# Kernel tuning notes

Hardware: AMD Instinct MI355X
Metric: run time of the kernel (lower is better)

## Reference

```python
import jax, jax.numpy as jnp
import numpy as np

EPS = 1e-06
H, D_MODEL = 16, 1024
DK = D_MODEL // H
B, S = 16, 4096


def elu_fea_map(x):
    return jax.nn.elu(x) + 1.0


def setup_inputs() -> dict:
    key = jax.random.key(0)
    ks = jax.random.split(key, 11)
    lim = 1.0 / np.sqrt(D_MODEL)
    u = lambda k, shp: jax.random.uniform(k, shp, jnp.float32, -lim, lim)
    return {
        "query": jax.random.normal(ks[0], (B, D_MODEL), jnp.float32),
        "key": jax.random.normal(ks[1], (B, S, D_MODEL), jnp.float32),
        "value": jax.random.normal(ks[2], (B, S, D_MODEL), jnp.float32),
        "Wq": u(ks[3], (D_MODEL, D_MODEL)), "bq": u(ks[4], (D_MODEL,)),
        "Wk": u(ks[5], (D_MODEL, D_MODEL)), "bk": u(ks[6], (D_MODEL,)),
        "Wv": u(ks[7], (D_MODEL, D_MODEL)), "bv": u(ks[8], (D_MODEL,)),
        "Wo": u(ks[9], (D_MODEL, D_MODEL)), "bo": u(ks[10], (D_MODEL,)),
    }


def reference(query, key, value, Wq, bq, Wk, bk, Wv, bv, Wo, bo):
    nb = query.shape[0]
    # projections; torch Linear: x @ W.T + b
    q = (query @ Wq.T + bq).reshape(nb, 1, H, DK)   # [B,1,H,D]
    k = (key @ Wk.T + bk).reshape(nb, -1, H, DK)    # [B,S,H,D]
    v = (value @ Wv.T + bv).reshape(nb, -1, H, DK)  # [B,S,H,M]
    Q = elu_fea_map(q)
    K = elu_fea_map(k)
    KV = jnp.einsum('bshd,bshm->bhdm', K, v)                      # [B,H,D,M]
    Z = 1.0 / (jnp.einsum('bshd,bhd->bsh', Q, K.sum(axis=1)) + EPS)  # [B,1,H]
    V = jnp.einsum('bshd,bhdm,bsh->bshm', Q, KV, Z)               # [B,1,H,M]
    x = V.reshape(nb, H * DK)
    return x @ Wo.T + bo
```

## Files before the change

### kernel.cpp

```cpp
#include <hip/hip_runtime.h>
#include <hip/hip_bf16.h>
#include <stdint.h>


using bf16 = __hip_bfloat16;
typedef __attribute__((ext_vector_type(8))) short short8;
typedef __attribute__((ext_vector_type(4))) float f32x4;

#define NB_B 16
#define SEQ 4096
#define DM 1024
#define NH 16
#define DKH 64

__device__ __forceinline__ void gload_lds16(const void* g, void* l) {
  __builtin_amdgcn_global_load_lds((const __attribute__((address_space(1))) void*)g,
                                   (__attribute__((address_space(3))) void*)l, 16, 0, 0);
}

__device__ __forceinline__ short8 pack_bf16x8(float4 a, float4 b) {
  union { bf16 h[8]; short8 v; } pk;
  pk.h[0] = __float2bfloat16(a.x); pk.h[1] = __float2bfloat16(a.y);
  pk.h[2] = __float2bfloat16(a.z); pk.h[3] = __float2bfloat16(a.w);
  pk.h[4] = __float2bfloat16(b.x); pk.h[5] = __float2bfloat16(b.y);
  pk.h[6] = __float2bfloat16(b.z); pk.h[7] = __float2bfloat16(b.w);
  return pk.v;
}

__global__ __launch_bounds__(256) void conv_kernel(const float* __restrict__ src,
                                                   bf16* __restrict__ dst, long n4) {
  long i = (long)blockIdx.x * blockDim.x + threadIdx.x;
  const long stride = (long)gridDim.x * blockDim.x;
  for (; i < n4; i += stride) {
    float4 v = ((const float4*)src)[i];
    union { ushort4 u; bf16 h[4]; } o;
    o.h[0] = __float2bfloat16(v.x);
    o.h[1] = __float2bfloat16(v.y);
    o.h[2] = __float2bfloat16(v.z);
    o.h[3] = __float2bfloat16(v.w);
    ((ushort4*)dst)[i] = o.u;
  }
}

template <int KPROJ>
__global__ __launch_bounds__(256) void gemm_proj(
    const float* __restrict__ A, const bf16* __restrict__ W,
    const float* __restrict__ bias, bf16* __restrict__ outT,
    float* __restrict__ Ksum, int rowsTot, int b0, int chunk) {
  __shared__ bf16 As[2][128 * 64];
  __shared__ bf16 Bs[2][128 * 64];
  const int tid = threadIdx.x;
  const int lane = tid & 63;
  const int wid = tid >> 6;
  const int wr = wid >> 1, wc = wid & 1;
  const int wgid = (blockIdx.x & 7) * chunk + (blockIdx.x >> 3);
  const int row0 = (wgid >> 3) * 128;
  const int col0 = (wgid & 7) * 128;
  f32x4 acc[4][4] = {};

  const int str = tid >> 3;
  const int sslotA = ((tid & 7) ^ (str & 7)) << 4;
  const int acol = (tid & 7) * 8;
  const int bsrc = ((lane & 7) ^ (lane >> 3)) * 8;
  const int xr = (lane & 7) << 4;
  const int lr = lane & 15;
  const int lk = (lane >> 4) * 16;

  const float* Arow[4];
#pragma unroll
  for (int i = 0; i < 4; ++i) Arow[i] = A + (long)(row0 + i * 32 + str) * DM + acol;
  const bf16* Wrow = W + (long)(col0 + wid * 32 + (lane >> 3)) * DM + bsrc;

  float4 fa[4][2];
#pragma unroll
  for (int i = 0; i < 4; ++i) {
    fa[i][0] = *(const float4*)(Arow[i]);
    fa[i][1] = *(const float4*)(Arow[i] + 4);
  }
#pragma unroll
  for (int i = 0; i < 4; ++i)
    gload_lds16(Wrow + i * 8 * DM, &Bs[0][(wid * 4 + i) * 512]);
#pragma unroll
  for (int i = 0; i < 4; ++i)
    *(short8*)((char*)As[0] + (i * 32 + str) * 128 + sslotA) = pack_bf16x8(fa[i][0], fa[i][1]);
#pragma unroll
  for (int i = 0; i < 4; ++i) {
    fa[i][0] = *(const float4*)(Arow[i] + 64);
    fa[i][1] = *(const float4*)(Arow[i] + 68);
  }
  asm volatile("s_waitcnt vmcnt(8) lgkmcnt(0)\n\ts_barrier" ::: "memory");
  __builtin_amdgcn_sched_barrier(0);

  for (int kt = 0; kt < 16; ++kt) {
    const int cur = kt & 1;
    bf16* Asc = As[cur];
    bf16* Bsc = Bs[cur];
    bf16* Asn = As[cur ^ 1];
    if (kt < 15) {
      const int kb = (kt + 1) * 64;
#pragma unroll
      for (int i = 0; i < 4; ++i)
        gload_lds16(Wrow + kb + i * 8 * DM, &Bs[cur ^ 1][(wid * 4 + i) * 512]);
    }
#pragma unroll
    for (int kk = 0; kk < 2; ++kk) {
      short8 af[4], bfv[4];
#pragma unroll
      for (int m = 0; m < 4; ++m)
        af[m] = *(const short8*)((char*)Asc + (wr * 64 + m * 16 + lr) * 128 + ((kk * 64 + lk) ^ xr));
#pragma unroll
      for (int n = 0; n < 4; ++n)
        bfv[n] = *(const short8*)((char*)Bsc + (wc * 64 + n * 16 + lr) * 128 + ((kk * 64 + lk) ^ xr));
#pragma unroll
      for (int m = 0; m < 4; ++m)
#pragma unroll
        for (int n = 0; n < 4; ++n)
          acc[m][n] = __builtin_amdgcn_mfma_f32_16x16x32_bf16(af[m], bfv[n], acc[m][n], 0, 0, 0);
    }
    if (kt < 15) {
#pragma unroll
      for (int i = 0; i < 4; ++i)
        *(short8*)((char*)Asn + (i * 32 + str) * 128 + sslotA) = pack_bf16x8(fa[i][0], fa[i][1]);
      if (kt < 14) {
        const int ka = (kt + 2) * 64;
#pragma unroll
        for (int i = 0; i < 4; ++i) {
          fa[i][0] = *(const float4*)(Arow[i] + ka);
          fa[i][1] = *(const float4*)(Arow[i] + ka + 4);
        }
        asm volatile("s_waitcnt vmcnt(8) lgkmcnt(0)\n\ts_barrier" ::: "memory");
      } else {
        asm volatile("s_waitcnt vmcnt(0) lgkmcnt(0)\n\ts_barrier" ::: "memory");
      }
      __builtin_amdgcn_sched_barrier(0);
    }
  }

  const int bglob = b0 + (row0 >> 12);
#pragma unroll
  for (int n = 0; n < 4; ++n) {
    const int colg = col0 + wc * 64 + n * 16 + (lane & 15);
    const float bv = bias[colg];
    float csum = 0.f;
#pragma unroll
    for (int m = 0; m < 4; ++m) {
      const int r = row0 + wr * 64 + m * 16 + (lane >> 4) * 4;
      union { ushort4 u; bf16 h[4]; } pk;
#pragma unroll
      for (int i = 0; i < 4; ++i) {
        float v = acc[m][n][i] + bv;
        if (KPROJ) { v = v > 0.f ? v + 1.f : __expf(v); csum += v; }
        pk.h[i] = __float2bfloat16(v);
      }
      *(ushort4*)&outT[(long)colg * rowsTot + r] = pk.u;
    }
    if (KPROJ) {
      csum += __shfl_xor(csum, 16);
      csum += __shfl_xor(csum, 32);
      if (lane < 16) atomicAdd(&Ksum[(long)bglob * DM + colg], csum);
    }
  }
}

__global__ __launch_bounds__(256) void kv_kernel(
    const bf16* __restrict__ KT, const bf16* __restrict__ VT,
    float* __restrict__ KVp, int rowsTot, int b0) {
  const int sp = blockIdx.x & 3;
  const int h = (blockIdx.x >> 2) & 15;
  const int b_loc = blockIdx.x >> 6;
  const int lane = threadIdx.x & 63;
  const int w = threadIdx.x >> 6;
  const long srow = (long)b_loc * SEQ + sp * (SEQ / 4) + ((lane >> 4) * 8);
  const bf16* Ab = KT + (long)(h * DKH + w * 16 + (lane & 15)) * rowsTot + srow;
  const bf16* Bb = VT + (long)(h * DKH + (lane & 15)) * rowsTot + srow;
  f32x4 acc[4] = {};
#pragma unroll 2
  for (int s = 0; s < SEQ / 4; s += 32) {
    short8 a = *(const short8*)(Ab + s);
#pragma unroll
    for (int n = 0; n < 4; ++n) {
      short8 bv = *(const short8*)(Bb + (long)n * 16 * rowsTot + s);
      acc[n] = __builtin_amdgcn_mfma_f32_16x16x32_bf16(a, bv, acc[n], 0, 0, 0);
    }
  }
  float* o = KVp + (((long)sp * NB_B + (b0 + b_loc)) * NH + h) * DKH * DKH;
#pragma unroll
  for (int n = 0; n < 4; ++n)
#pragma unroll
    for (int i = 0; i < 4; ++i)
      o[(w * 16 + (lane >> 4) * 4 + i) * DKH + n * 16 + (lane & 15)] = acc[n][i];
}

template <int ELU>
__global__ __launch_bounds__(256) void vecmat_kernel(
    const float* __restrict__ in, const float* __restrict__ W,
    const float* __restrict__ bias, float* __restrict__ outp) {
  const int b = blockIdx.x >> 5;
  const int n0 = (blockIdx.x & 31) * 32;
  const int lane = threadIdx.x & 63;
  const int w = threadIdx.x >> 6;
  float4 qv[4];
#pragma unroll
  for (int it = 0; it < 4; ++it)
    qv[it] = *(const float4*)&in[(long)b * DM + it * 256 + lane * 4];
#pragma unroll
  for (int j = 0; j < 8; ++j) {
    const int n = n0 + w * 8 + j;
    const float* wrow = W + (long)n * DM;
    float s = 0.f;
#pragma unroll
    for (int it = 0; it < 4; ++it) {
      float4 wv = *(const float4*)&wrow[it * 256 + lane * 4];
      s += qv[it].x * wv.x + qv[it].y * wv.y + qv[it].z * wv.z + qv[it].w * wv.w;
    }
    s += __shfl_xor(s, 1);  s += __shfl_xor(s, 2);  s += __shfl_xor(s, 4);
    s += __shfl_xor(s, 8);  s += __shfl_xor(s, 16); s += __shfl_xor(s, 32);
    if (lane == 0) {
      float v = s + bias[n];
      if (ELU) v = v > 0.f ? v + 1.f : __expf(v);
      outp[(long)b * DM + n] = v;
    }
  }
}

__global__ __launch_bounds__(256) void xcomp_kernel(
    const float* __restrict__ Q, const float* __restrict__ KVp,
    const float* __restrict__ Ksum, float* __restrict__ xb) {
  const int b = blockIdx.x;
  const int t = threadIdx.x;
  const int h = t >> 4;
  const int m0 = (t & 15) * 4;
  const float* q = Q + (long)b * DM + h * DKH;
  const float* ks = Ksum + (long)b * DM + h * DKH;
  const long kvoff = ((long)b * NH + h) * DKH * DKH;
  const long spstride = (long)NB_B * NH * DKH * DKH;
  float zden = 0.f;
#pragma unroll
  for (int d = 0; d < DKH; ++d) zden += q[d] * ks[d];
  const float z = 1.f / (zden + 1e-6f);
  float nv[4] = {0.f, 0.f, 0.f, 0.f};
  for (int d = 0; d < DKH; ++d) {
    const float qd = q[d];
#pragma unroll
    for (int j = 0; j < 4; ++j) {
      const long idx = kvoff + d * DKH + m0 + j;
      nv[j] += qd * (KVp[idx] + KVp[idx + spstride] +
                     KVp[idx + 2 * spstride] + KVp[idx + 3 * spstride]);
    }
  }
  float* xo = xb + (long)b * DM + h * DKH + m0;
#pragma unroll
  for (int j = 0; j < 4; ++j) xo[j] = nv[j] * z;
}

extern "C" void kernel_launch(void* const* d_in, const int* in_sizes, int n_in,
                              void* d_out, int out_size, void* d_ws, size_t ws_size,
                              hipStream_t stream) {
  (void)in_sizes; (void)n_in; (void)out_size;
  const float* query = (const float*)d_in[0];
  const float* key   = (const float*)d_in[1];
  const float* value = (const float*)d_in[2];
  const float* Wq = (const float*)d_in[3];
  const float* bq = (const float*)d_in[4];
  const float* Wk = (const float*)d_in[5];
  const float* bk = (const float*)d_in[6];
  const float* Wv = (const float*)d_in[7];
  const float* bv = (const float*)d_in[8];
  const float* Wo = (const float*)d_in[9];
  const float* bo = (const float*)d_in[10];
  float* out = (float*)d_out;

  char* p = (char*)d_ws;
  bf16* WkB = (bf16*)p;  p += (size_t)DM * DM * 2;
  bf16* WvB = (bf16*)p;  p += (size_t)DM * DM * 2;
  float* KVp = (float*)p; p += (size_t)4 * NB_B * NH * DKH * DKH * 4;
  float* Ksum = (float*)p; p += (size_t)NB_B * DM * 4;
  float* Q = (float*)p;  p += (size_t)NB_B * DM * 4;
  float* xb = (float*)p; p += (size_t)NB_B * DM * 4;
  const size_t fixed = (size_t)(p - (char*)d_ws);
  const size_t per_b = (size_t)2 * SEQ * DM * 2;
  if (ws_size < fixed + per_b) return;
  int nbc = (int)((ws_size - fixed) / per_b);
  if (nbc > NB_B) nbc = NB_B;
  bf16* kT = (bf16*)p; p += (size_t)nbc * SEQ * DM * 2;
  bf16* vT = (bf16*)p; p += (size_t)nbc * SEQ * DM * 2;

  hipMemsetAsync(Ksum, 0, (size_t)NB_B * DM * 4, stream);
  conv_kernel<<<512, 256, 0, stream>>>(Wk, WkB, (long)DM * DM / 4);
  conv_kernel<<<512, 256, 0, stream>>>(Wv, WvB, (long)DM * DM / 4);
  vecmat_kernel<1><<<NB_B * 32, 256, 0, stream>>>(query, Wq, bq, Q);

  for (int b0 = 0; b0 < NB_B; b0 += nbc) {
    const int nb = (NB_B - b0 < nbc) ? (NB_B - b0) : nbc;
    const int rows = nb * SEQ;
    const int nwg = (rows / 128) * 8;
    gemm_proj<1><<<nwg, 256, 0, stream>>>(key + (size_t)b0 * SEQ * DM, WkB, bk, kT, Ksum, rows, b0, nwg / 8);
    gemm_proj<0><<<nwg, 256, 0, stream>>>(value + (size_t)b0 * SEQ * DM, WvB, bv, vT, (float*)nullptr, rows, b0, nwg / 8);
    kv_kernel<<<nb * NH * 4, 256, 0, stream>>>(kT, vT, KVp, rows, b0);
  }

  xcomp_kernel<<<NB_B, 256, 0, stream>>>(Q, KVp, Ksum, xb);
  vecmat_kernel<0><<<NB_B * 32, 256, 0, stream>>>(xb, Wo, bo, out);
}
```

Before: 641.5 us.

## Pre-convert activations to bf16 and use 256x256 GEMM tiles with phased MFMA schedule

Key and value inputs are now converted from fp32 to bf16 by separate passes. The projection GEMMs then load both operands straight into LDS through global_load_lds, and the GEMM tile grows from 128x128 to 256x256 with 8 waves, split into barrier-separated phases that raise wave priority around the MFMA blocks. The aim is more operand reuse per tile and no in-loop fp32-to-bf16 packing. The cost is an extra full read of the fp32 activations plus a bf16 write and reread, and a workspace that doubles per batch, which may shrink the batch chunk size.

Measured after the change: 683.8 us. 6.6% more time.

```diff
diff --git a/kernel.cpp b/kernel.cpp
--- a/kernel.cpp
+++ b/kernel.cpp
@@ -16,15 +16,6 @@
 __device__ __forceinline__ void gload_lds16(const void* g, void* l) {
   __builtin_amdgcn_global_load_lds((const __attribute__((address_space(1))) void*)g,
                                    (__attribute__((address_space(3))) void*)l, 16, 0, 0);
-}
-
-__device__ __forceinline__ short8 pack_bf16x8(float4 a, float4 b) {
-  union { bf16 h[8]; short8 v; } pk;
-  pk.h[0] = __float2bfloat16(a.x); pk.h[1] = __float2bfloat16(a.y);
-  pk.h[2] = __float2bfloat16(a.z); pk.h[3] = __float2bfloat16(a.w);
-  pk.h[4] = __float2bfloat16(b.x); pk.h[5] = __float2bfloat16(b.y);
-  pk.h[6] = __float2bfloat16(b.z); pk.h[7] = __float2bfloat16(b.w);
-  return pk.v;
 }
 
 __global__ __launch_bounds__(256) void conv_kernel(const float* __restrict__ src,
@@ -43,108 +34,134 @@
 }
 
 template <int KPROJ>
-__global__ __launch_bounds__(256) void gemm_proj(
-    const float* __restrict__ A, const bf16* __restrict__ W,
+__global__ __launch_bounds__(512, 1) void gemm256(
+    const bf16* __restrict__ A, const bf16* __restrict__ W,
     const float* __restrict__ bias, bf16* __restrict__ outT,
     float* __restrict__ Ksum, int rowsTot, int b0, int chunk) {
-  __shared__ bf16 As[2][128 * 64];
-  __shared__ bf16 Bs[2][128 * 64];
+  __shared__ bf16 As[2][256 * 64];
+  __shared__ bf16 Bs[2][256 * 64];
   const int tid = threadIdx.x;
   const int lane = tid & 63;
   const int wid = tid >> 6;
-  const int wr = wid >> 1, wc = wid & 1;
+  const int wr = wid >> 2;
+  const int wc = wid & 3;
   const int wgid = (blockIdx.x & 7) * chunk + (blockIdx.x >> 3);
-  const int row0 = (wgid >> 3) * 128;
-  const int col0 = (wgid & 7) * 128;
-  f32x4 acc[4][4] = {};
-
-  const int str = tid >> 3;
-  const int sslotA = ((tid & 7) ^ (str & 7)) << 4;
-  const int acol = (tid & 7) * 8;
+  const int row0 = (wgid >> 2) * 256;
+  const int col0 = (wgid & 3) * 256;
+
+  f32x4 acc[8][4] = {};
+
   const int bsrc = ((lane & 7) ^ (lane >> 3)) * 8;
   const int xr = (lane & 7) << 4;
   const int lr = lane & 15;
   const int lk = (lane >> 4) * 16;
 
-  const float* Arow[4];
-#pragma unroll
-  for (int i = 0; i < 4; ++i) Arow[i] = A + (long)(row0 + i * 32 + str) * DM + acol;
-  const bf16* Wrow = W + (long)(col0 + wid * 32 + (lane >> 3)) * DM + bsrc;
-
-  float4 fa[4][2];
-#pragma unroll
-  for (int i = 0; i < 4; ++i) {
-    fa[i][0] = *(const float4*)(Arow[i]);
-    fa[i][1] = *(const float4*)(Arow[i] + 4);
-  }
-#pragma unroll
-  for (int i = 0; i < 4; ++i)
-    gload_lds16(Wrow + i * 8 * DM, &Bs[0][(wid * 4 + i) * 512]);
-#pragma unroll
-  for (int i = 0; i < 4; ++i)
-    *(short8*)((char*)As[0] + (i * 32 + str) * 128 + sslotA) = pack_bf16x8(fa[i][0], fa[i][1]);
-#pragma unroll
-  for (int i = 0; i < 4; ++i) {
-    fa[i][0] = *(const float4*)(Arow[i] + 64);
-    fa[i][1] = *(const float4*)(Arow[i] + 68);
-  }
-  asm volatile("s_waitcnt vmcnt(8) lgkmcnt(0)\n\ts_barrier" ::: "memory");
-  __builtin_amdgcn_sched_barrier(0);
+  const bf16* Ab = A + (long)(row0 + wid * 32 + (lane >> 3)) * DM + bsrc;
+  const bf16* Wb = W + (long)(col0 + wid * 32 + (lane >> 3)) * DM + bsrc;
+  const int sdst = (wid * 32) * 64;
+
+#pragma unroll
+  for (int j = 0; j < 4; ++j)
+    gload_lds16(Ab + (long)j * 8 * DM, (void*)&As[0][sdst + j * 512]);
+#pragma unroll
+  for (int j = 0; j < 4; ++j)
+    gload_lds16(Wb + (long)j * 8 * DM, (void*)&Bs[0][sdst + j * 512]);
+  asm volatile("s_waitcnt vmcnt(0)\n\ts_barrier" ::: "memory");
+
+  short8 af[4], bfv[4];
 
   for (int kt = 0; kt < 16; ++kt) {
     const int cur = kt & 1;
-    bf16* Asc = As[cur];
-    bf16* Bsc = Bs[cur];
+    const char* Asc = (const char*)As[cur];
+    const char* Bsc = (const char*)Bs[cur];
     bf16* Asn = As[cur ^ 1];
+    bf16* Bsn = Bs[cur ^ 1];
+    const long kbn = (kt + 1) * 64;
+
     if (kt < 15) {
-      const int kb = (kt + 1) * 64;
-#pragma unroll
-      for (int i = 0; i < 4; ++i)
-        gload_lds16(Wrow + kb + i * 8 * DM, &Bs[cur ^ 1][(wid * 4 + i) * 512]);
-    }
-#pragma unroll
-    for (int kk = 0; kk < 2; ++kk) {
-      short8 af[4], bfv[4];
-#pragma unroll
-      for (int m = 0; m < 4; ++m)
-        af[m] = *(const short8*)((char*)Asc + (wr * 64 + m * 16 + lr) * 128 + ((kk * 64 + lk) ^ xr));
+#pragma unroll
+      for (int j = 0; j < 4; ++j)
+        gload_lds16(Ab + (long)j * 8 * DM + kbn, (void*)&Asn[sdst + j * 512]);
+      asm volatile("s_waitcnt vmcnt(4)\n\ts_barrier" ::: "memory");
+    } else {
+      asm volatile("s_waitcnt vmcnt(0)\n\ts_barrier" ::: "memory");
+    }
+#pragma unroll
+    for (int m = 0; m < 4; ++m)
+      af[m] = *(const short8*)(Asc + (wr * 128 + m * 16 + lr) * 128 + (lk ^ xr));
+#pragma unroll
+    for (int n = 0; n < 4; ++n)
+      bfv[n] = *(const short8*)(Bsc + (wc * 64 + n * 16 + lr) * 128 + (lk ^ xr));
+    __builtin_amdgcn_sched_barrier(0);
+    __builtin_amdgcn_s_setprio(1);
+#pragma unroll
+    for (int m = 0; m < 4; ++m)
 #pragma unroll
       for (int n = 0; n < 4; ++n)
-        bfv[n] = *(const short8*)((char*)Bsc + (wc * 64 + n * 16 + lr) * 128 + ((kk * 64 + lk) ^ xr));
-#pragma unroll
-      for (int m = 0; m < 4; ++m)
-#pragma unroll
-        for (int n = 0; n < 4; ++n)
-          acc[m][n] = __builtin_amdgcn_mfma_f32_16x16x32_bf16(af[m], bfv[n], acc[m][n], 0, 0, 0);
-    }
+        acc[m][n] = __builtin_amdgcn_mfma_f32_16x16x32_bf16(af[m], bfv[n], acc[m][n], 0, 0, 0);
+    __builtin_amdgcn_s_setprio(0);
+    asm volatile("s_barrier" ::: "memory");
+
+#pragma unroll
+    for (int m = 0; m < 4; ++m)
+      af[m] = *(const short8*)(Asc + (wr * 128 + (m + 4) * 16 + lr) * 128 + (lk ^ xr));
     if (kt < 15) {
 #pragma unroll
-      for (int i = 0; i < 4; ++i)
-        *(short8*)((char*)Asn + (i * 32 + str) * 128 + sslotA) = pack_bf16x8(fa[i][0], fa[i][1]);
-      if (kt < 14) {
-        const int ka = (kt + 2) * 64;
-#pragma unroll
-        for (int i = 0; i < 4; ++i) {
-          fa[i][0] = *(const float4*)(Arow[i] + ka);
-          fa[i][1] = *(const float4*)(Arow[i] + ka + 4);
-        }
-        asm volatile("s_waitcnt vmcnt(8) lgkmcnt(0)\n\ts_barrier" ::: "memory");
-      } else {
-        asm volatile("s_waitcnt vmcnt(0) lgkmcnt(0)\n\ts_barrier" ::: "memory");
-      }
-      __builtin_amdgcn_sched_barrier(0);
-    }
+      for (int j = 0; j < 4; ++j)
+        gload_lds16(Wb + (long)j * 8 * DM + kbn, (void*)&Bsn[sdst + j * 512]);
+    }
+    asm volatile("s_barrier" ::: "memory");
+    __builtin_amdgcn_sched_barrier(0);
+    __builtin_amdgcn_s_setprio(1);
+#pragma unroll
+    for (int m = 0; m < 4; ++m)
+#pragma unroll
+      for (int n = 0; n < 4; ++n)
+        acc[m + 4][n] = __builtin_amdgcn_mfma_f32_16x16x32_bf16(af[m], bfv[n], acc[m + 4][n], 0, 0, 0);
+    __builtin_amdgcn_s_setprio(0);
+    asm volatile("s_barrier" ::: "memory");
+
+#pragma unroll
+    for (int m = 0; m < 4; ++m)
+      af[m] = *(const short8*)(Asc + (wr * 128 + m * 16 + lr) * 128 + ((64 + lk) ^ xr));
+#pragma unroll
+    for (int n = 0; n < 4; ++n)
+      bfv[n] = *(const short8*)(Bsc + (wc * 64 + n * 16 + lr) * 128 + ((64 + lk) ^ xr));
+    asm volatile("s_barrier" ::: "memory");
+    __builtin_amdgcn_sched_barrier(0);
+    __builtin_amdgcn_s_setprio(1);
+#pragma unroll
+    for (int m = 0; m < 4; ++m)
+#pragma unroll
+      for (int n = 0; n < 4; ++n)
+        acc[m][n] = __builtin_amdgcn_mfma_f32_16x16x32_bf16(af[m], bfv[n], acc[m][n], 0, 0, 0);
+    __builtin_amdgcn_s_setprio(0);
+    asm volatile("s_barrier" ::: "memory");
+
+#pragma unroll
+    for (int m = 0; m < 4; ++m)
+      af[m] = *(const short8*)(Asc + (wr * 128 + (m + 4) * 16 + lr) * 128 + ((64 + lk) ^ xr));
+    asm volatile("s_barrier" ::: "memory");
+    __builtin_amdgcn_sched_barrier(0);
+    __builtin_amdgcn_s_setprio(1);
+#pragma unroll
+    for (int m = 0; m < 4; ++m)
+#pragma unroll
+      for (int n = 0; n < 4; ++n)
+        acc[m + 4][n] = __builtin_amdgcn_mfma_f32_16x16x32_bf16(af[m], bfv[n], acc[m + 4][n], 0, 0, 0);
+    __builtin_amdgcn_s_setprio(0);
+    asm volatile("s_barrier" ::: "memory");
   }
 
   const int bglob = b0 + (row0 >> 12);
 #pragma unroll
   for (int n = 0; n < 4; ++n) {
-    const int colg = col0 + wc * 64 + n * 16 + (lane & 15);
+    const int colg = col0 + wc * 64 + n * 16 + lr;
     const float bv = bias[colg];
     float csum = 0.f;
 #pragma unroll
-    for (int m = 0; m < 4; ++m) {
-      const int r = row0 + wr * 64 + m * 16 + (lane >> 4) * 4;
+    for (int m = 0; m < 8; ++m) {
+      const int r = row0 + wr * 128 + m * 16 + (lane >> 4) * 4;
       union { ushort4 u; bf16 h[4]; } pk;
 #pragma unroll
       for (int i = 0; i < 4; ++i) {
@@ -278,12 +295,14 @@
   float* Q = (float*)p;  p += (size_t)NB_B * DM * 4;
   float* xb = (float*)p; p += (size_t)NB_B * DM * 4;
   const size_t fixed = (size_t)(p - (char*)d_ws);
-  const size_t per_b = (size_t)2 * SEQ * DM * 2;
+  const size_t per_b = (size_t)4 * SEQ * DM * 2;
   if (ws_size < fixed + per_b) return;
   int nbc = (int)((ws_size - fixed) / per_b);
   if (nbc > NB_B) nbc = NB_B;
-  bf16* kT = (bf16*)p; p += (size_t)nbc * SEQ * DM * 2;
-  bf16* vT = (bf16*)p; p += (size_t)nbc * SEQ * DM * 2;
+  bf16* keyB = (bf16*)p; p += (size_t)nbc * SEQ * DM * 2;
+  bf16* valB = (bf16*)p; p += (size_t)nbc * SEQ * DM * 2;
+  bf16* kT   = (bf16*)p; p += (size_t)nbc * SEQ * DM * 2;
+  bf16* vT   = (bf16*)p; p += (size_t)nbc * SEQ * DM * 2;
 
   hipMemsetAsync(Ksum, 0, (size_t)NB_B * DM * 4, stream);
   conv_kernel<<<512, 256, 0, stream>>>(Wk, WkB, (long)DM * DM / 4);
@@ -293,9 +312,12 @@
   for (int b0 = 0; b0 < NB_B; b0 += nbc) {
     const int nb = (NB_B - b0 < nbc) ? (NB_B - b0) : nbc;
     const int rows = nb * SEQ;
-    const int nwg = (rows / 128) * 8;
-    gemm_proj<1><<<nwg, 256, 0, stream>>>(key + (size_t)b0 * SEQ * DM, WkB, bk, kT, Ksum, rows, b0, nwg / 8);
-    gemm_proj<0><<<nwg, 256, 0, stream>>>(value + (size_t)b0 * SEQ * DM, WvB, bv, vT, (float*)nullptr, rows, b0, nwg / 8);
+    const long n4 = (long)rows * DM / 4;
+    conv_kernel<<<2048, 256, 0, stream>>>(key + (size_t)b0 * SEQ * DM, keyB, n4);
+    conv_kernel<<<2048, 256, 0, stream>>>(value + (size_t)b0 * SEQ * DM, valB, n4);
+    const int nwg = (rows / 256) * 4;
+    gemm256<1><<<nwg, 512, 0, stream>>>(keyB, WkB, bk, kT, Ksum, rows, b0, nwg / 8);
+    gemm256<0><<<nwg, 512, 0, stream>>>(valB, WvB, bv, vT, (float*)nullptr, rows, b0, nwg / 8);
     kv_kernel<<<nb * NH * 4, 256, 0, stream>>>(kT, vT, KVp, rows, b0);
   }
 
```
